# Kernel optimization log

Measured on AMD Instinct MI355X. Metric: run time of the kernel, lower is better.

The kernel has to match this reference:

```python
import jax, jax.numpy as jnp
import numpy as np
import math

N, M = 512, 31
INP, EMB, ATT = 64, 64, 64
NUM_RELS = 200
SELF_LOOP_IDX = NUM_RELS  # index num_rels is the self-loop relation


def setup_inputs() -> dict:
    key = jax.random.key(0)
    ks = jax.random.split(key, 11)
    s_w = 1.0 / math.sqrt(EMB)
    return {
        "h": jax.random.normal(ks[0], (N, INP), jnp.float32),
        "msg": jax.random.normal(ks[1], (N, M, EMB), jnp.float32),
        "msg_type": jax.random.randint(ks[2], (N, M), 0, NUM_RELS, jnp.int32),
        "r_label_node": jax.random.randint(ks[3], (N,), 0, NUM_RELS, jnp.int32),
        "r_label_msg": jax.random.randint(ks[4], (N, M), 0, NUM_RELS, jnp.int32),
        "W_self": jax.random.normal(ks[5], (INP, EMB), jnp.float32) * s_w,
        "Q": jax.random.normal(ks[6], (NUM_RELS + 1, EMB, ATT), jnp.float32) * s_w,
        "K": jax.random.normal(ks[7], (NUM_RELS + 1, EMB, ATT), jnp.float32) * s_w,
        "V": jax.random.normal(ks[8], (NUM_RELS + 1, EMB, ATT), jnp.float32) * s_w,
        "ffn_w": jax.random.normal(ks[9], (ATT, EMB), jnp.float32) * s_w,
        "ffn_b": jnp.zeros((EMB,), jnp.float32),
    }


def reference(h, msg, msg_type, r_label_node, r_label_msg, W_self, Q, K, V, ffn_w, ffn_b):
    curr = h @ W_self                                        # [N, EMB]
    x = jnp.concatenate([curr[:, None, :], msg], axis=1)     # [N, M+1, EMB]
    qv_idx = jnp.concatenate([r_label_node[:, None], r_label_msg], axis=1)  # [N, M+1]
    self_col = jnp.full((x.shape[0], 1), SELF_LOOP_IDX, msg_type.dtype)
    k_idx = jnp.concatenate([self_col, msg_type], axis=1)    # [N, M+1]
    # relation-indexed per-token projection weights (irregular gather)
    q = jnp.einsum("nme,nmea->nma", x, Q[qv_idx])            # [N, M+1, ATT]
    k = jnp.einsum("nme,nmea->nma", x, K[k_idx])             # [N, M+1, ATT]
    v = jnp.einsum("nme,nmea->nma", x, V[qv_idx])            # [N, M+1, ATT]
    scores = jnp.einsum("nqa,nka->nqk", q, k) / math.sqrt(ATT)
    # NOTE: original code applies softmax over dim=1 (the query axis)
    att = jax.nn.softmax(scores, axis=1)                     # [N, M+1, M+1]
    pooled = jnp.einsum("nqk,nka->nqa", att, v)[:, 0]        # [N, ATT]
    return pooled @ ffn_w + ffn_b                            # [N, EMB]
```

## Files before the change

### kernel.cpp

```cpp
#include <hip/hip_runtime.h>
#include <math.h>

#define NN 512
#define MM 31
#define TT 32
#define EE 64
#define STR 68
#define SELF_LOOP 200

__global__ __launch_bounds__(256) void transpool_kernel(
    const float* __restrict__ h,
    const float* __restrict__ msg,
    const int*   __restrict__ msg_type,
    const int*   __restrict__ r_label_node,
    const int*   __restrict__ r_label_msg,
    const float* __restrict__ W_self,
    const float* __restrict__ Q,
    const float* __restrict__ K,
    const float* __restrict__ V,
    const float* __restrict__ ffn_w,
    const float* __restrict__ ffn_b,
    float* __restrict__ out)
{
    const int n   = blockIdx.x;
    const int tid = threadIdx.x;

    __shared__ float x_s[TT][STR];
    __shared__ float q_s[TT][STR];
    __shared__ float k_s[TT][STR];
    __shared__ float v_s[TT][STR];
    __shared__ float s_s[TT][TT + 1];
    __shared__ float att0[TT];
    __shared__ float pooled[EE];
    __shared__ int   qv_s[TT];
    __shared__ int   kx_s[TT];

    if (tid < TT) {
        qv_s[tid] = (tid == 0) ? r_label_node[n] : r_label_msg[n * MM + tid - 1];
        kx_s[tid] = (tid == 0) ? SELF_LOOP      : msg_type[n * MM + tid - 1];
    }

    {
        const float4* msg4 = (const float4*)(msg + (size_t)n * MM * EE);
        for (int i4 = tid; i4 < MM * EE / 4; i4 += 256) {
            int m = i4 >> 4, c = i4 & 15;
            ((float4*)&x_s[1 + m][0])[c] = msg4[i4];
        }
    }

    if (tid < EE) {
        float acc = 0.f;
        const float* hrow = h + n * EE;
        for (int e = 0; e < EE; ++e)
            acc = fmaf(hrow[e], W_self[e * EE + tid], acc);
        x_s[0][tid] = acc;
    }
    __syncthreads();

    {
        const int a16 = tid & 15;
        const int mo  = tid >> 4;
        for (int mg = 0; mg < TT; mg += 16) {
            int m  = mg + mo;
            int rq = qv_s[m];
            int rk = kx_s[m];
            const float4* Qp = (const float4*)(Q + (size_t)rq * EE * EE) + a16;
            const float4* Kp = (const float4*)(K + (size_t)rk * EE * EE) + a16;
            const float4* Vp = (const float4*)(V + (size_t)rq * EE * EE) + a16;
            float4 qa = {0, 0, 0, 0}, ka = {0, 0, 0, 0}, va = {0, 0, 0, 0};
            for (int e = 0; e < EE; ++e) {
                float  xe = x_s[m][e];
                float4 qw = Qp[(size_t)e * 16];
                float4 kw = Kp[(size_t)e * 16];
                float4 vw = Vp[(size_t)e * 16];
                qa.x = fmaf(xe, qw.x, qa.x); qa.y = fmaf(xe, qw.y, qa.y);
                qa.z = fmaf(xe, qw.z, qa.z); qa.w = fmaf(xe, qw.w, qa.w);
                ka.x = fmaf(xe, kw.x, ka.x); ka.y = fmaf(xe, kw.y, ka.y);
                ka.z = fmaf(xe, kw.z, ka.z); ka.w = fmaf(xe, kw.w, ka.w);
                va.x = fmaf(xe, vw.x, va.x); va.y = fmaf(xe, vw.y, va.y);
                va.z = fmaf(xe, vw.z, va.z); va.w = fmaf(xe, vw.w, va.w);
            }
            ((float4*)&q_s[m][0])[a16] = qa;
            ((float4*)&k_s[m][0])[a16] = ka;
            ((float4*)&v_s[m][0])[a16] = va;
        }
    }
    __syncthreads();

    {
        const int ki = tid & 31;
        for (int qi = tid >> 5; qi < TT; qi += 8) {
            const float4* qp = (const float4*)&q_s[qi][0];
            const float4* kp = (const float4*)&k_s[ki][0];
            float acc = 0.f;
            for (int e4 = 0; e4 < EE / 4; ++e4) {
                float4 a = qp[e4], b = kp[e4];
                acc += a.x * b.x + a.y * b.y + a.z * b.z + a.w * b.w;
            }
            s_s[qi][ki] = acc * 0.125f;
        }
    }
    __syncthreads();

    if (tid < TT) {
        float mx = -INFINITY;
        for (int qi = 0; qi < TT; ++qi) mx = fmaxf(mx, s_s[qi][tid]);
        float sum = 0.f;
        for (int qi = 0; qi < TT; ++qi) sum += __expf(s_s[qi][tid] - mx);
        att0[tid] = __expf(s_s[0][tid] - mx) / sum;
    }
    __syncthreads();

    if (tid < EE) {
        float acc = 0.f;
        for (int ki = 0; ki < TT; ++ki)
            acc = fmaf(att0[ki], v_s[ki][tid], acc);
        pooled[tid] = acc;
    }
    __syncthreads();

    if (tid < EE) {
        float acc = ffn_b[tid];
        for (int a = 0; a < EE; ++a)
            acc = fmaf(pooled[a], ffn_w[a * EE + tid], acc);
        out[n * EE + tid] = acc;
    }
}

extern "C" void kernel_launch(void* const* d_in, const int* in_sizes, int n_in,
                              void* d_out, int out_size, void* d_ws, size_t ws_size,
                              hipStream_t stream) {
    const float* h            = (const float*)d_in[0];
    const float* msg          = (const float*)d_in[1];
    const int*   msg_type     = (const int*)  d_in[2];
    const int*   r_label_node = (const int*)  d_in[3];
    const int*   r_label_msg  = (const int*)  d_in[4];
    const float* W_self       = (const float*)d_in[5];
    const float* Q            = (const float*)d_in[6];
    const float* K            = (const float*)d_in[7];
    const float* V            = (const float*)d_in[8];
    const float* ffn_w        = (const float*)d_in[9];
    const float* ffn_b        = (const float*)d_in[10];
    float*       out          = (float*)d_out;

    transpool_kernel<<<NN, 256, 0, stream>>>(h, msg, msg_type, r_label_node,
                                             r_label_msg, W_self, Q, K, V,
                                             ffn_w, ffn_b, out);
}
```

Before: 126.6 us.

## Group tokens by relation and project with shared-memory weights per relation

The single fused kernel is split into three kernels: a prep kernel that computes the self projection and its self-loop key, a per-relation projection kernel, and an attention kernel. The projection kernel runs one block per relation. Each block scans all labels to build lists of the tokens that use that relation, loads the relation's Q/V and K matrices into shared memory once, and computes projections for 64 tokens at a time with register tiling. This replaces a scattered per-token global weight gather with reuse of staged weights. In exchange it adds two extra launches, a workspace round trip for q/k/v, and a full label scan in each of the 200 blocks. The lists are capped at 1024 entries, so a heavily skewed label distribution would silently drop tokens.

```diff
diff --git a/kernel.cpp b/kernel.cpp
--- a/kernel.cpp
+++ b/kernel.cpp
@@ -5,84 +5,227 @@
 #define MM 31
 #define TT 32
 #define EE 64
-#define STR 68
+#define NREL 200
 #define SELF_LOOP 200
-
-__global__ __launch_bounds__(256) void transpool_kernel(
-    const float* __restrict__ h,
-    const float* __restrict__ msg,
-    const int*   __restrict__ msg_type,
-    const int*   __restrict__ r_label_node,
-    const int*   __restrict__ r_label_msg,
-    const float* __restrict__ W_self,
-    const float* __restrict__ Q,
+#define LCAP 1024
+
+__global__ __launch_bounds__(64) void prep_kernel(
+    const float* __restrict__ h, const float* __restrict__ W_self,
     const float* __restrict__ K,
+    float* __restrict__ curr_all, float* __restrict__ k_all)
+{
+    const int n = blockIdx.x, a = threadIdx.x;
+    __shared__ float c_s[EE];
+    const float* hrow = h + n * EE;
+    float acc = 0.f;
+#pragma unroll 8
+    for (int e = 0; e < EE; ++e)
+        acc = fmaf(hrow[e], W_self[e * EE + a], acc);
+    curr_all[n * EE + a] = acc;
+    c_s[a] = acc;
+    __syncthreads();
+    const float* K200 = K + (size_t)SELF_LOOP * EE * EE;
+    float k0 = 0.f;
+#pragma unroll 8
+    for (int e = 0; e < EE; ++e)
+        k0 = fmaf(c_s[e], K200[e * EE + a], k0);
+    k_all[(size_t)n * TT * EE + a] = k0;
+}
+
+__global__ __launch_bounds__(256) void proj_kernel(
+    const float* __restrict__ curr_all, const float* __restrict__ msg,
+    const int* __restrict__ msg_type, const int* __restrict__ r_label_node,
+    const int* __restrict__ r_label_msg,
+    const float* __restrict__ Q, const float* __restrict__ K,
     const float* __restrict__ V,
-    const float* __restrict__ ffn_w,
-    const float* __restrict__ ffn_b,
-    float* __restrict__ out)
+    float* __restrict__ q_all, float* __restrict__ k_all,
+    float* __restrict__ v_all)
 {
-    const int n   = blockIdx.x;
+    const int r   = blockIdx.x;
     const int tid = threadIdx.x;
 
-    __shared__ float x_s[TT][STR];
-    __shared__ float q_s[TT][STR];
-    __shared__ float k_s[TT][STR];
-    __shared__ float v_s[TT][STR];
+    __shared__ float wA[4096];
+    __shared__ float wB[4096];
+    __shared__ float x_s[64][68];
+    __shared__ int   list_q[LCAP], list_k[LCAP];
+    __shared__ int   nq_s, nk_s;
+
+    if (tid == 0) { nq_s = 0; nk_s = 0; }
+    __syncthreads();
+
+    for (int i = tid; i < NN; i += 256)
+        if (r_label_node[i] == r) {
+            int p = atomicAdd(&nq_s, 1);
+            if (p < LCAP) list_q[p] = i * TT;
+        }
+    for (int j = tid; j < NN * MM; j += 256) {
+        int rl = r_label_msg[j];
+        int mt = msg_type[j];
+        if (rl == r) {
+            int n = j / MM, m = j - n * MM;
+            int p = atomicAdd(&nq_s, 1);
+            if (p < LCAP) list_q[p] = n * TT + m + 1;
+        }
+        if (mt == r) {
+            int n = j / MM, m = j - n * MM;
+            int p = atomicAdd(&nk_s, 1);
+            if (p < LCAP) list_k[p] = n * TT + m + 1;
+        }
+    }
+
+    {
+        const float4* Qs = (const float4*)(Q + (size_t)r * EE * EE);
+        const float4* Vs = (const float4*)(V + (size_t)r * EE * EE);
+        for (int i = tid; i < 1024; i += 256) {
+            ((float4*)wA)[i] = Qs[i];
+            ((float4*)wB)[i] = Vs[i];
+        }
+    }
+    __syncthreads();
+
+    const int nq = min(nq_s, LCAP);
+    const int nk = min(nk_s, LCAP);
+    const int oc  = tid & 15;
+    const int tr4 = (tid >> 4) * 4;
+
+    for (int base = 0; base < nq; base += 64) {
+        {
+            int tl = tid >> 2;
+            int idx = base + tl;
+            if (idx < nq) {
+                int token = list_q[idx];
+                int n = token >> 5, t = token & 31;
+                const float4* src = (t == 0)
+                    ? (const float4*)(curr_all + n * EE)
+                    : (const float4*)(msg + ((size_t)n * MM + (t - 1)) * EE);
+#pragma unroll
+                for (int p = 0; p < 4; ++p) {
+                    int fc = (tid & 3) + 4 * p;
+                    ((float4*)&x_s[tl][0])[fc] = src[fc];
+                }
+            }
+        }
+        __syncthreads();
+
+        float4 aq[4], av[4];
+#pragma unroll
+        for (int i = 0; i < 4; ++i) { aq[i] = make_float4(0,0,0,0); av[i] = make_float4(0,0,0,0); }
+
+#pragma unroll 4
+        for (int e = 0; e < EE; ++e) {
+            float4 wq4 = ((const float4*)wA)[e * 16 + oc];
+            float4 wv4 = ((const float4*)wB)[e * 16 + oc];
+            float x0 = x_s[tr4 + 0][e];
+            float x1 = x_s[tr4 + 1][e];
+            float x2 = x_s[tr4 + 2][e];
+            float x3 = x_s[tr4 + 3][e];
+            aq[0].x = fmaf(x0, wq4.x, aq[0].x); aq[0].y = fmaf(x0, wq4.y, aq[0].y);
+            aq[0].z = fmaf(x0, wq4.z, aq[0].z); aq[0].w = fmaf(x0, wq4.w, aq[0].w);
+            aq[1].x = fmaf(x1, wq4.x, aq[1].x); aq[1].y = fmaf(x1, wq4.y, aq[1].y);
+            aq[1].z = fmaf(x1, wq4.z, aq[1].z); aq[1].w = fmaf(x1, wq4.w, aq[1].w);
+            aq[2].x = fmaf(x2, wq4.x, aq[2].x); aq[2].y = fmaf(x2, wq4.y, aq[2].y);
+            aq[2].z = fmaf(x2, wq4.z, aq[2].z); aq[2].w = fmaf(x2, wq4.w, aq[2].w);
+            aq[3].x = fmaf(x3, wq4.x, aq[3].x); aq[3].y = fmaf(x3, wq4.y, aq[3].y);
+            aq[3].z = fmaf(x3, wq4.z, aq[3].z); aq[3].w = fmaf(x3, wq4.w, aq[3].w);
+            av[0].x = fmaf(x0, wv4.x, av[0].x); av[0].y = fmaf(x0, wv4.y, av[0].y);
+            av[0].z = fmaf(x0, wv4.z, av[0].z); av[0].w = fmaf(x0, wv4.w, av[0].w);
+            av[1].x = fmaf(x1, wv4.x, av[1].x); av[1].y = fmaf(x1, wv4.y, av[1].y);
+            av[1].z = fmaf(x1, wv4.z, av[1].z); av[1].w = fmaf(x1, wv4.w, av[1].w);
+            av[2].x = fmaf(x2, wv4.x, av[2].x); av[2].y = fmaf(x2, wv4.y, av[2].y);
+            av[2].z = fmaf(x2, wv4.z, av[2].z); av[2].w = fmaf(x2, wv4.w, av[2].w);
+            av[3].x = fmaf(x3, wv4.x, av[3].x); av[3].y = fmaf(x3, wv4.y, av[3].y);
+            av[3].z = fmaf(x3, wv4.z, av[3].z); av[3].w = fmaf(x3, wv4.w, av[3].w);
+        }
+
+#pragma unroll
+        for (int i = 0; i < 4; ++i) {
+            int idx = base + tr4 + i;
+            if (idx < nq) {
+                int token = list_q[idx];
+                ((float4*)(q_all + (size_t)token * EE))[oc] = aq[i];
+                ((float4*)(v_all + (size_t)token * EE))[oc] = av[i];
+            }
+        }
+        __syncthreads();
+    }
+
+    {
+        const float4* Ks = (const float4*)(K + (size_t)r * EE * EE);
+        for (int i = tid; i < 1024; i += 256)
+            ((float4*)wA)[i] = Ks[i];
+    }
+    __syncthreads();
+
+    for (int base = 0; base < nk; base += 64) {
+        {
+            int tl = tid >> 2;
+            int idx = base + tl;
+            if (idx < nk) {
+                int token = list_k[idx];
+                int n = token >> 5, t = token & 31;
+                const float4* src = (const float4*)(msg + ((size_t)n * MM + (t - 1)) * EE);
+#pragma unroll
+                for (int p = 0; p < 4; ++p) {
+                    int fc = (tid & 3) + 4 * p;
+                    ((float4*)&x_s[tl][0])[fc] = src[fc];
+                }
+            }
+        }
+        __syncthreads();
+
+        float4 ak[4];
+#pragma unroll
+        for (int i = 0; i < 4; ++i) ak[i] = make_float4(0,0,0,0);
+
+#pragma unroll 4
+        for (int e = 0; e < EE; ++e) {
+            float4 wk4 = ((const float4*)wA)[e * 16 + oc];
+            float x0 = x_s[tr4 + 0][e];
+            float x1 = x_s[tr4 + 1][e];
+            float x2 = x_s[tr4 + 2][e];
+            float x3 = x_s[tr4 + 3][e];
+            ak[0].x = fmaf(x0, wk4.x, ak[0].x); ak[0].y = fmaf(x0, wk4.y, ak[0].y);
+            ak[0].z = fmaf(x0, wk4.z, ak[0].z); ak[0].w = fmaf(x0, wk4.w, ak[0].w);
+            ak[1].x = fmaf(x1, wk4.x, ak[1].x); ak[1].y = fmaf(x1, wk4.y, ak[1].y);
+            ak[1].z = fmaf(x1, wk4.z, ak[1].z); ak[1].w = fmaf(x1, wk4.w, ak[1].w);
+            ak[2].x = fmaf(x2, wk4.x, ak[2].x); ak[2].y = fmaf(x2, wk4.y, ak[2].y);
+            ak[2].z = fmaf(x2, wk4.z, ak[2].z); ak[2].w = fmaf(x2, wk4.w, ak[2].w);
+            ak[3].x = fmaf(x3, wk4.x, ak[3].x); ak[3].y = fmaf(x3, wk4.y, ak[3].y);
+            ak[3].z = fmaf(x3, wk4.z, ak[3].z); ak[3].w = fmaf(x3, wk4.w, ak[3].w);
+        }
+
+#pragma unroll
+        for (int i = 0; i < 4; ++i) {
+            int idx = base + tr4 + i;
+            if (idx < nk) {
+                int token = list_k[idx];
+                ((float4*)(k_all + (size_t)token * EE))[oc] = ak[i];
+            }
+        }
+        __syncthreads();
+    }
+}
+
+__global__ __launch_bounds__(256) void attn_kernel(
+    const float* __restrict__ q_all, const float* __restrict__ k_all,
+    const float* __restrict__ v_all, const float* __restrict__ ffn_w,
+    const float* __restrict__ ffn_b, float* __restrict__ out)
+{
+    const int n = blockIdx.x, tid = threadIdx.x;
+    __shared__ float q_s[TT][68], k_s[TT][68], v_s[TT][68];
     __shared__ float s_s[TT][TT + 1];
     __shared__ float att0[TT];
     __shared__ float pooled[EE];
-    __shared__ int   qv_s[TT];
-    __shared__ int   kx_s[TT];
-
-    if (tid < TT) {
-        qv_s[tid] = (tid == 0) ? r_label_node[n] : r_label_msg[n * MM + tid - 1];
-        kx_s[tid] = (tid == 0) ? SELF_LOOP      : msg_type[n * MM + tid - 1];
-    }
-
-    {
-        const float4* msg4 = (const float4*)(msg + (size_t)n * MM * EE);
-        for (int i4 = tid; i4 < MM * EE / 4; i4 += 256) {
-            int m = i4 >> 4, c = i4 & 15;
-            ((float4*)&x_s[1 + m][0])[c] = msg4[i4];
-        }
-    }
-
-    if (tid < EE) {
-        float acc = 0.f;
-        const float* hrow = h + n * EE;
-        for (int e = 0; e < EE; ++e)
-            acc = fmaf(hrow[e], W_self[e * EE + tid], acc);
-        x_s[0][tid] = acc;
-    }
-    __syncthreads();
-
-    {
-        const int a16 = tid & 15;
-        const int mo  = tid >> 4;
-        for (int mg = 0; mg < TT; mg += 16) {
-            int m  = mg + mo;
-            int rq = qv_s[m];
-            int rk = kx_s[m];
-            const float4* Qp = (const float4*)(Q + (size_t)rq * EE * EE) + a16;
-            const float4* Kp = (const float4*)(K + (size_t)rk * EE * EE) + a16;
-            const float4* Vp = (const float4*)(V + (size_t)rq * EE * EE) + a16;
-            float4 qa = {0, 0, 0, 0}, ka = {0, 0, 0, 0}, va = {0, 0, 0, 0};
-            for (int e = 0; e < EE; ++e) {
-                float  xe = x_s[m][e];
-                float4 qw = Qp[(size_t)e * 16];
-                float4 kw = Kp[(size_t)e * 16];
-                float4 vw = Vp[(size_t)e * 16];
-                qa.x = fmaf(xe, qw.x, qa.x); qa.y = fmaf(xe, qw.y, qa.y);
-                qa.z = fmaf(xe, qw.z, qa.z); qa.w = fmaf(xe, qw.w, qa.w);
-                ka.x = fmaf(xe, kw.x, ka.x); ka.y = fmaf(xe, kw.y, ka.y);
-                ka.z = fmaf(xe, kw.z, ka.z); ka.w = fmaf(xe, kw.w, ka.w);
-                va.x = fmaf(xe, vw.x, va.x); va.y = fmaf(xe, vw.y, va.y);
-                va.z = fmaf(xe, vw.z, va.z); va.w = fmaf(xe, vw.w, va.w);
-            }
-            ((float4*)&q_s[m][0])[a16] = qa;
-            ((float4*)&k_s[m][0])[a16] = ka;
-            ((float4*)&v_s[m][0])[a16] = va;
+
+    {
+        const float4* qg = (const float4*)(q_all + (size_t)n * TT * EE);
+        const float4* kg = (const float4*)(k_all + (size_t)n * TT * EE);
+        const float4* vg = (const float4*)(v_all + (size_t)n * TT * EE);
+        for (int i = tid; i < TT * EE / 4; i += 256) {
+            int row = i >> 4, col = i & 15;
+            ((float4*)&q_s[row][0])[col] = qg[i];
+            ((float4*)&k_s[row][0])[col] = kg[i];
+            ((float4*)&v_s[row][0])[col] = vg[i];
         }
     }
     __syncthreads();
@@ -143,7 +286,14 @@
     const float* ffn_b        = (const float*)d_in[10];
     float*       out          = (float*)d_out;
 
-    transpool_kernel<<<NN, 256, 0, stream>>>(h, msg, msg_type, r_label_node,
-                                             r_label_msg, W_self, Q, K, V,
-                                             ffn_w, ffn_b, out);
-}
+    float* curr_all = (float*)d_ws;
+    float* q_all = curr_all + NN * EE;
+    float* k_all = q_all + (size_t)NN * TT * EE;
+    float* v_all = k_all + (size_t)NN * TT * EE;
+
+    prep_kernel<<<NN, 64, 0, stream>>>(h, W_self, K, curr_all, k_all);
+    proj_kernel<<<NREL, 256, 0, stream>>>(curr_all, msg, msg_type, r_label_node,
+                                          r_label_msg, Q, K, V,
+                                          q_all, k_all, v_all);
+    attn_kernel<<<NN, 256, 0, stream>>>(q_all, k_all, v_all, ffn_w, ffn_b, out);
+}
```

New measurement: 134.8 us. +6.5%, slower.
